# Kernel tuning notes

Measured on AMD Instinct MI355X. Metric: run time of the kernel, lower is better.

The kernel has to match this reference:

```python
import jax, jax.numpy as jnp
import numpy as np

B, N, D = 2, 8192, 1024
H, DH = 8, 64  # heads, dim_head; inner = H*DH = 512
INNER = H * DH


def setup_inputs() -> dict:
    key = jax.random.key(0)
    k1, k2, k3 = jax.random.split(key, 3)
    x = jax.random.normal(k1, (B, N, D), dtype=jnp.float32)
    # xavier_uniform-ish scaling for weights
    W_qkv = jax.random.normal(k2, (D, 3 * INNER), dtype=jnp.float32) * (1.0 / np.sqrt(D))
    W_out = jax.random.normal(k3, (INNER, D), dtype=jnp.float32) * (1.0 / np.sqrt(INNER))
    b_out = jnp.zeros((D,), dtype=jnp.float32)
    return {"x": x, "W_qkv": W_qkv, "W_out": W_out, "b_out": b_out}


def reference(x, W_qkv, W_out, b_out):
    b, n, d = x.shape
    qkv = x @ W_qkv                               # [b, n, 3*inner]
    q, k, v = jnp.split(qkv, 3, axis=-1)          # each [b, n, inner]

    def to_heads(t):
        return t.reshape(b, n, H, DH).transpose(0, 2, 1, 3)  # [b, h, n, dh]

    q, k, v = to_heads(q), to_heads(k), to_heads(v)
    q = jax.nn.softmax(q, axis=-1)                # over dim_head
    k = jax.nn.softmax(k, axis=-2)                # over sequence
    # context: k^T v  -> [b, h, dh, dh]
    context = jnp.einsum('bhnd,bhne->bhde', k, v)
    out = jnp.einsum('bhnd,bhde->bhne', q, context)  # [b, h, n, dh]
    out = out.transpose(0, 2, 1, 3).reshape(b, n, INNER)
    return out @ W_out + b_out                    # [b, n, d]
```

## Files before the change

### kernel.cpp

```cpp
#include <hip/hip_runtime.h>
#include <stdint.h>


typedef _Float16 half4 __attribute__((ext_vector_type(4)));
typedef _Float16 half8 __attribute__((ext_vector_type(8)));
typedef float f32x4 __attribute__((ext_vector_type(4)));

#define WS_XB 0UL
#define WS_WQKVT 33554432UL
#define WS_CWT 37748736UL
#define WS_EKH 54525952UL
#define WS_VH 71303168UL
#define WS_SQ 88080384UL
#define WS_CTXPART 104857600UL
#define WS_COLPART 113246208UL

__device__ __forceinline__ void gld16(const void* g, void* l) {
  __builtin_amdgcn_global_load_lds(
      (const __attribute__((address_space(1))) unsigned int*)g,
      (__attribute__((address_space(3))) unsigned int*)l, 16, 0, 0);
}

__global__ void prep_kernel(const float* __restrict__ x,
                            const float* __restrict__ Wqkv,
                            _Float16* __restrict__ xb,
                            _Float16* __restrict__ wqkvT) {
  const int blk = blockIdx.x;
  if (blk < 16384) {
    int i = blk * 256 + threadIdx.x;
    f32x4 v = *(const f32x4*)(x + (size_t)i * 4);
    half4 h = {(_Float16)v[0], (_Float16)v[1], (_Float16)v[2], (_Float16)v[3]};
    *(half4*)(xb + (size_t)i * 4) = h;
  } else {
    int i = (blk - 16384) * 256 + threadIdx.x;
    int c = i >> 10, r = i & 1023;
    wqkvT[i] = (_Float16)Wqkv[(size_t)r * 1536 + c];
  }
}


__device__ __forceinline__ void stage_tile(const _Float16* __restrict__ G, int K,
                                           int rowbase, int kt, char* region,
                                           int t) {
  char* wbase = region + (t & ~63) * 16;
#pragma unroll
  for (int q = 0; q < 4; ++q) {
    const int row = q * 32 + (t >> 3);
    const int col8 = ((t & 7) ^ (row & 7)) * 8;
    gld16(G + (size_t)(rowbase + row) * K + kt + col8, wbase + q * 4096);
  }
}

template <int EPI>
__global__ __launch_bounds__(256, 2) void gemm128(
    const _Float16* __restrict__ A, const _Float16* __restrict__ BT, int K,
    int NTN, int bstride, _Float16* __restrict__ oQ, _Float16* __restrict__ oK,
    _Float16* __restrict__ oV, float* __restrict__ oC,
    const float* __restrict__ bias) {
  __shared__ char lds[65536];
  const int t = threadIdx.x;
  const int l = t & 63, w = t >> 6;
  const int wm = w >> 1, wn = w & 1;
  const int fr = l & 15, qq = l >> 4;
  const int swzx = (fr & 7) << 4;

  const int nwg = gridDim.x;
  const int cpx = nwg >> 3;
  const int wg = (blockIdx.x & 7) * cpx + (blockIdx.x >> 3);
  const int tileM = wg / NTN, tileN = wg - tileM * NTN;
  const int mbase = tileM * 128, nbase = tileN * 128;
  BT += (size_t)(tileM >> 6) * bstride;

  const int NT = K >> 6;
  f32x4 acc[4][4] = {};
  half8 a[4][2], b[4][2];

  auto STG = [&](int tile) {
    int kt = tile * 64;
    if (kt > K - 64) kt = K - 64;
    char* base = lds + ((tile & 1) << 15);
    stage_tile(A, K, mbase, kt, base, t);
    stage_tile(BT, K, nbase, kt, base + 16384, t);
  };

  STG(0);
  STG(1);
  asm volatile("s_waitcnt vmcnt(8)" ::: "memory");
  __builtin_amdgcn_s_barrier();

  for (int t2 = 0; t2 < NT; ++t2) {
    const char* ldsA = lds + ((t2 & 1) << 15);
    const char* ldsB = ldsA + 16384;
    STG(t2 + 1);
#pragma unroll
    for (int mi = 0; mi < 4; ++mi)
#pragma unroll
      for (int kk = 0; kk < 2; ++kk) {
        int off = (wm * 64 + mi * 16 + fr) * 128 + ((kk * 64 + qq * 16) ^ swzx);
        a[mi][kk] = *(const half8*)(ldsA + off);
      }
#pragma unroll
    for (int ni = 0; ni < 4; ++ni)
#pragma unroll
      for (int kk = 0; kk < 2; ++kk) {
        int off = (wn * 64 + ni * 16 + fr) * 128 + ((kk * 64 + qq * 16) ^ swzx);
        b[ni][kk] = *(const half8*)(ldsB + off);
      }
    __builtin_amdgcn_s_barrier();
    __builtin_amdgcn_s_setprio(1);
#pragma unroll
    for (int mi = 0; mi < 4; ++mi)
#pragma unroll
      for (int ni = 0; ni < 2; ++ni)
#pragma unroll
        for (int kk = 0; kk < 2; ++kk)
          acc[mi][ni] = __builtin_amdgcn_mfma_f32_16x16x32_f16(
              a[mi][kk], b[ni][kk], acc[mi][ni], 0, 0, 0);
    __builtin_amdgcn_s_setprio(0);
    asm volatile("s_waitcnt vmcnt(0) lgkmcnt(0)" ::: "memory");
    __builtin_amdgcn_s_barrier();
    __builtin_amdgcn_s_setprio(1);
#pragma unroll
    for (int mi = 0; mi < 4; ++mi)
#pragma unroll
      for (int ni = 2; ni < 4; ++ni)
#pragma unroll
        for (int kk = 0; kk < 2; ++kk)
          acc[mi][ni] = __builtin_amdgcn_mfma_f32_16x16x32_f16(
              a[mi][kk], b[ni][kk], acc[mi][ni], 0, 0, 0);
    __builtin_amdgcn_s_setprio(0);
  }

  if (EPI == 0) {
    const int gcol0 = nbase + wn * 64;
    const int which = gcol0 >> 9;
    if (which == 0) {
#pragma unroll
      for (int mi = 0; mi < 4; ++mi) {
        const int grow = mbase + wm * 64 + mi * 16 + qq * 4;
        float e[4][4], rs[4];
#pragma unroll
        for (int r = 0; r < 4; ++r) {
          float s = 0.f;
#pragma unroll
          for (int ni = 0; ni < 4; ++ni) {
            e[ni][r] = __expf(acc[mi][ni][r]);
            s += e[ni][r];
          }
#pragma unroll
          for (int off = 1; off < 16; off <<= 1) s += __shfl_xor(s, off, 64);
          rs[r] = 1.f / s;
        }
#pragma unroll
        for (int ni = 0; ni < 4; ++ni) {
          const int gcol = gcol0 + ni * 16 + fr;
#pragma unroll
          for (int r = 0; r < 4; ++r)
            oQ[(size_t)(grow + r) * 512 + gcol] = (_Float16)(e[ni][r] * rs[r]);
        }
      }
    } else {
      _Float16* dst0 = (which == 1) ? oK : oV;
      const int h = (gcol0 >> 6) & 7;
#pragma unroll
      for (int mi = 0; mi < 4; ++mi) {
        const int grow = mbase + wm * 64 + mi * 16 + qq * 4;
        const int bidx = grow >> 13, n = grow & 8191;
        const size_t rb = ((size_t)((bidx << 3) + h) * 8192 + n) * 64;
#pragma unroll
        for (int ni = 0; ni < 4; ++ni) {
          const int d = ni * 16 + fr;
#pragma unroll
          for (int r = 0; r < 4; ++r) {
            float v = acc[mi][ni][r];
            if (which == 1) v = __expf(v);
            dst0[rb + (size_t)r * 64 + d] = (_Float16)v;
          }
        }
      }
    }
  } else {
#pragma unroll
    for (int mi = 0; mi < 4; ++mi) {
      const int grow = mbase + wm * 64 + mi * 16 + qq * 4;
#pragma unroll
      for (int ni = 0; ni < 4; ++ni) {
        const int gcol = nbase + wn * 64 + ni * 16 + fr;
        const float bb = bias[gcol];
#pragma unroll
        for (int r = 0; r < 4; ++r)
          oC[(size_t)(grow + r) * 1024 + gcol] = acc[mi][ni][r] + bb;
      }
    }
  }
}

__global__ __launch_bounds__(256, 2) void ctx_partial_kernel(
    const _Float16* __restrict__ ekh, const _Float16* __restrict__ vh,
    float* __restrict__ ctxpart, float* __restrict__ colpart) {
  __shared__ char smem[65536];
  __shared__ float credu[4][64];
  _Float16* sek = (_Float16*)smem;
  _Float16* svv = (_Float16*)(smem + 32768);
  const int t = threadIdx.x, l = t & 63, w = t >> 6;
  const int bh = blockIdx.x >> 5, ch = blockIdx.x & 31;
  const size_t rowbase = ((size_t)bh * 8192 + ch * 256) * 64;
  {
    const char* eksrc = (const char*)(ekh + rowbase);
    const char* vsrc = (const char*)(vh + rowbase);
    char* ekbase = smem + w * 1024;
    char* vbase = smem + 32768 + w * 1024;
#pragma unroll
    for (int s = 0; s < 8; ++s) {
      gld16(eksrc + (size_t)(s * 256 + t) * 16, ekbase + s * 4096);
      gld16(vsrc + (size_t)(s * 256 + t) * 16, vbase + s * 4096);
    }
  }
  asm volatile("s_waitcnt vmcnt(0)" ::: "memory");
  __builtin_amdgcn_s_barrier();

  const int d0 = (l & 7) * 8, e0 = (l >> 3) * 8;
  f32x4 acc[8][2] = {};
  float cacc[8] = {};
  const int n0 = w * 64;
  for (int n = n0; n < n0 + 64; ++n) {
    half8 k8 = *(const half8*)&sek[n * 64 + d0];
    half8 v8 = *(const half8*)&svv[n * 64 + e0];
    float e[8];
    f32x4 v4[2];
#pragma unroll
    for (int i = 0; i < 8; ++i) e[i] = (float)k8[i];
#pragma unroll
    for (int j = 0; j < 8; ++j) v4[j >> 2][j & 3] = (float)v8[j];
#pragma unroll
    for (int i = 0; i < 8; ++i) {
      cacc[i] += e[i];
      acc[i][0] += v4[0] * e[i];
      acc[i][1] += v4[1] * e[i];
    }
  }
  __builtin_amdgcn_s_barrier();
  float* red = (float*)smem;
#pragma unroll
  for (int i = 0; i < 8; ++i) {
    *(f32x4*)&red[w * 4096 + (d0 + i) * 64 + e0] = acc[i][0];
    *(f32x4*)&red[w * 4096 + (d0 + i) * 64 + e0 + 4] = acc[i][1];
  }
  if (l < 8) {
#pragma unroll
    for (int i = 0; i < 8; ++i) credu[w][l * 8 + i] = cacc[i];
  }
  __syncthreads();
  float* cp = ctxpart + (size_t)blockIdx.x * 4096;
#pragma unroll
  for (int s = 0; s < 4; ++s) {
    const int r = t * 16 + s * 4;
    f32x4 sum = *(const f32x4*)&red[r];
    sum += *(const f32x4*)&red[4096 + r];
    sum += *(const f32x4*)&red[8192 + r];
    sum += *(const f32x4*)&red[12288 + r];
    *(f32x4*)&cp[r] = sum;
  }
  if (t < 64)
    colpart[blockIdx.x * 64 + t] =
        credu[0][t] + credu[1][t] + credu[2][t] + credu[3][t];
}

__global__ __launch_bounds__(256) void ctxw_kernel(
    const float* __restrict__ ctxpart, const float* __restrict__ colpart,
    const float* __restrict__ Wout, _Float16* __restrict__ cwT) {
  __shared__ float part[4][64];
  __shared__ float csp[32];
  __shared__ float crow[64];
  const int blk = blockIdx.x;
  const int bh = blk >> 6, d = blk & 63;
  const int b = bh >> 3, h = bh & 7;
  const int t = threadIdx.x;
  const int e = t & 63, cq = t >> 6;
  float p = 0.f;
#pragma unroll
  for (int cc = 0; cc < 8; ++cc)
    p += ctxpart[(size_t)(bh * 32 + cq * 8 + cc) * 4096 + d * 64 + e];
  part[cq][e] = p;
  if (t >= 64 && t < 96)
    csp[t - 64] = colpart[(size_t)(bh * 32 + (t - 64)) * 64 + d];
  __syncthreads();
  if (t < 64) {
    float csum = 0.f;
#pragma unroll
    for (int c = 0; c < 32; ++c) csum += csp[c];
    crow[t] = (part[0][t] + part[1][t] + part[2][t] + part[3][t]) / csum;
  }
  __syncthreads();
  float acc[4] = {};
  for (int e2 = 0; e2 < 64; ++e2) {
    const float c = crow[e2];
    const float* wr = Wout + (size_t)(h * 64 + e2) * 1024 + t;
#pragma unroll
    for (int j = 0; j < 4; ++j) acc[j] += c * wr[j * 256];
  }
  _Float16* dst = cwT + (size_t)b * 524288 + (size_t)t * 512 + h * 64 + d;
#pragma unroll
  for (int j = 0; j < 4; ++j) dst[(size_t)j * 256 * 512] = (_Float16)acc[j];
}

extern "C" void kernel_launch(void* const* d_in, const int* in_sizes, int n_in,
                              void* d_out, int out_size, void* d_ws, size_t ws_size,
                              hipStream_t stream) {
  const float* x = (const float*)d_in[0];
  const float* Wqkv = (const float*)d_in[1];
  const float* Wout = (const float*)d_in[2];
  const float* bout = (const float*)d_in[3];
  float* out = (float*)d_out;
  char* ws = (char*)d_ws;

  _Float16* xb = (_Float16*)(ws + WS_XB);
  _Float16* wqkvT = (_Float16*)(ws + WS_WQKVT);
  _Float16* cwT = (_Float16*)(ws + WS_CWT);
  _Float16* ekh = (_Float16*)(ws + WS_EKH);
  _Float16* vh = (_Float16*)(ws + WS_VH);
  _Float16* sq = (_Float16*)(ws + WS_SQ);
  float* ctxpart = (float*)(ws + WS_CTXPART);
  float* colpart = (float*)(ws + WS_COLPART);

  prep_kernel<<<22528, 256, 0, stream>>>(x, Wqkv, xb, wqkvT);
  gemm128<0><<<1536, 256, 0, stream>>>(xb, wqkvT, 1024, 12, 0, sq, ekh, vh,
                                       nullptr, nullptr);
  ctx_partial_kernel<<<512, 256, 0, stream>>>(ekh, vh, ctxpart, colpart);
  ctxw_kernel<<<1024, 256, 0, stream>>>(ctxpart, colpart, Wout, cwT);
  gemm128<1><<<1024, 256, 0, stream>>>(sq, cwT, 512, 8, 524288, nullptr,
                                       nullptr, nullptr, out, bout);
}
```

Before: 162.6 us.

## Fuse K^T V context partials into QKV GEMM epilogue

```diff
diff --git a/kernel.cpp b/kernel.cpp
--- a/kernel.cpp
+++ b/kernel.cpp
@@ -9,11 +9,9 @@
 #define WS_XB 0UL
 #define WS_WQKVT 33554432UL
 #define WS_CWT 37748736UL
-#define WS_EKH 54525952UL
-#define WS_VH 71303168UL
+#define WS_CTXPART 54525952UL
+#define WS_COLPART 71303168UL
 #define WS_SQ 88080384UL
-#define WS_CTXPART 104857600UL
-#define WS_COLPART 113246208UL
 
 __device__ __forceinline__ void gld16(const void* g, void* l) {
   __builtin_amdgcn_global_load_lds(
@@ -51,12 +49,24 @@
   }
 }
 
+__device__ __forceinline__ void stage_tile64(const _Float16* __restrict__ G,
+                                             int K, int rowbase, int kt,
+                                             char* region, int t) {
+  char* wbase = region + (t & ~63) * 16;
+#pragma unroll
+  for (int q = 0; q < 2; ++q) {
+    const int row = q * 32 + (t >> 3);
+    const int col8 = ((t & 7) ^ (row & 7)) * 8;
+    gld16(G + (size_t)(rowbase + row) * K + kt + col8, wbase + q * 4096);
+  }
+}
+
 template <int EPI>
 __global__ __launch_bounds__(256, 2) void gemm128(
     const _Float16* __restrict__ A, const _Float16* __restrict__ BT, int K,
-    int NTN, int bstride, _Float16* __restrict__ oQ, _Float16* __restrict__ oK,
-    _Float16* __restrict__ oV, float* __restrict__ oC,
-    const float* __restrict__ bias) {
+    int NTN, int bstride, _Float16* __restrict__ oQ,
+    float* __restrict__ ctxpart, float* __restrict__ colpart,
+    float* __restrict__ oC, const float* __restrict__ bias) {
   __shared__ char lds[65536];
   const int t = threadIdx.x;
   const int l = t & 63, w = t >> 6;
@@ -80,7 +90,13 @@
     if (kt > K - 64) kt = K - 64;
     char* base = lds + ((tile & 1) << 15);
     stage_tile(A, K, mbase, kt, base, t);
-    stage_tile(BT, K, nbase, kt, base + 16384, t);
+    if (EPI == 1 || tileN < 4) {
+      stage_tile(BT, K, nbase, kt, base + 16384, t);
+    } else {
+      const int h = tileN - 4;
+      stage_tile64(BT, K, 512 + h * 64, kt, base + 16384, t);
+      stage_tile64(BT, K, 1024 + h * 64, kt, base + 16384 + 8192, t);
+    }
   };
 
   STG(0);
@@ -132,9 +148,8 @@
   }
 
   if (EPI == 0) {
-    const int gcol0 = nbase + wn * 64;
-    const int which = gcol0 >> 9;
-    if (which == 0) {
+    if (tileN < 4) {
+      const int gcol0 = nbase + wn * 64;
 #pragma unroll
       for (int mi = 0; mi < 4; ++mi) {
         const int grow = mbase + wm * 64 + mi * 16 + qq * 4;
@@ -160,24 +175,44 @@
         }
       }
     } else {
-      _Float16* dst0 = (which == 1) ? oK : oV;
-      const int h = (gcol0 >> 6) & 7;
+      const int h = tileN - 4;
+      float* sf = (float*)lds;
 #pragma unroll
       for (int mi = 0; mi < 4; ++mi) {
-        const int grow = mbase + wm * 64 + mi * 16 + qq * 4;
-        const int bidx = grow >> 13, n = grow & 8191;
-        const size_t rb = ((size_t)((bidx << 3) + h) * 8192 + n) * 64;
+        const int n = wm * 64 + mi * 16 + qq * 4;
 #pragma unroll
         for (int ni = 0; ni < 4; ++ni) {
-          const int d = ni * 16 + fr;
+          const int c = wn * 64 + ni * 16 + fr;
 #pragma unroll
           for (int r = 0; r < 4; ++r) {
             float v = acc[mi][ni][r];
-            if (which == 1) v = __expf(v);
-            dst0[rb + (size_t)r * 64 + d] = (_Float16)v;
+            if (wn == 0) v = __expf(v);
+            sf[(size_t)(n + r) * 128 + c] = v;
           }
         }
       }
+      __syncthreads();
+      const int d0 = (t & 15) * 4, e0 = (t >> 4) * 4;
+      f32x4 cacc = {0.f, 0.f, 0.f, 0.f};
+      float pacc[4][4] = {};
+      for (int n = 0; n < 128; ++n) {
+        f32x4 ek4 = *(const f32x4*)&sf[(size_t)n * 128 + d0];
+        f32x4 vv4 = *(const f32x4*)&sf[(size_t)n * 128 + 64 + e0];
+        cacc += ek4;
+#pragma unroll
+        for (int i = 0; i < 4; ++i)
+#pragma unroll
+          for (int j = 0; j < 4; ++j) pacc[i][j] += ek4[i] * vv4[j];
+      }
+      const int bh = (tileM >> 6) * 8 + h, chunk = tileM & 63;
+      float* cp = ctxpart + ((size_t)bh * 64 + chunk) * 4096;
+#pragma unroll
+      for (int i = 0; i < 4; ++i) {
+        f32x4 o = {pacc[i][0], pacc[i][1], pacc[i][2], pacc[i][3]};
+        *(f32x4*)&cp[(d0 + i) * 64 + e0] = o;
+      }
+      if (t < 16)
+        *(f32x4*)&colpart[((size_t)bh * 64 + chunk) * 64 + d0] = cacc;
     }
   } else {
 #pragma unroll
@@ -193,84 +228,13 @@
       }
     }
   }
-}
-
-__global__ __launch_bounds__(256, 2) void ctx_partial_kernel(
-    const _Float16* __restrict__ ekh, const _Float16* __restrict__ vh,
-    float* __restrict__ ctxpart, float* __restrict__ colpart) {
-  __shared__ char smem[65536];
-  __shared__ float credu[4][64];
-  _Float16* sek = (_Float16*)smem;
-  _Float16* svv = (_Float16*)(smem + 32768);
-  const int t = threadIdx.x, l = t & 63, w = t >> 6;
-  const int bh = blockIdx.x >> 5, ch = blockIdx.x & 31;
-  const size_t rowbase = ((size_t)bh * 8192 + ch * 256) * 64;
-  {
-    const char* eksrc = (const char*)(ekh + rowbase);
-    const char* vsrc = (const char*)(vh + rowbase);
-    char* ekbase = smem + w * 1024;
-    char* vbase = smem + 32768 + w * 1024;
-#pragma unroll
-    for (int s = 0; s < 8; ++s) {
-      gld16(eksrc + (size_t)(s * 256 + t) * 16, ekbase + s * 4096);
-      gld16(vsrc + (size_t)(s * 256 + t) * 16, vbase + s * 4096);
-    }
-  }
-  asm volatile("s_waitcnt vmcnt(0)" ::: "memory");
-  __builtin_amdgcn_s_barrier();
-
-  const int d0 = (l & 7) * 8, e0 = (l >> 3) * 8;
-  f32x4 acc[8][2] = {};
-  float cacc[8] = {};
-  const int n0 = w * 64;
-  for (int n = n0; n < n0 + 64; ++n) {
-    half8 k8 = *(const half8*)&sek[n * 64 + d0];
-    half8 v8 = *(const half8*)&svv[n * 64 + e0];
-    float e[8];
-    f32x4 v4[2];
-#pragma unroll
-    for (int i = 0; i < 8; ++i) e[i] = (float)k8[i];
-#pragma unroll
-    for (int j = 0; j < 8; ++j) v4[j >> 2][j & 3] = (float)v8[j];
-#pragma unroll
-    for (int i = 0; i < 8; ++i) {
-      cacc[i] += e[i];
-      acc[i][0] += v4[0] * e[i];
-      acc[i][1] += v4[1] * e[i];
-    }
-  }
-  __builtin_amdgcn_s_barrier();
-  float* red = (float*)smem;
-#pragma unroll
-  for (int i = 0; i < 8; ++i) {
-    *(f32x4*)&red[w * 4096 + (d0 + i) * 64 + e0] = acc[i][0];
-    *(f32x4*)&red[w * 4096 + (d0 + i) * 64 + e0 + 4] = acc[i][1];
-  }
-  if (l < 8) {
-#pragma unroll
-    for (int i = 0; i < 8; ++i) credu[w][l * 8 + i] = cacc[i];
-  }
-  __syncthreads();
-  float* cp = ctxpart + (size_t)blockIdx.x * 4096;
-#pragma unroll
-  for (int s = 0; s < 4; ++s) {
-    const int r = t * 16 + s * 4;
-    f32x4 sum = *(const f32x4*)&red[r];
-    sum += *(const f32x4*)&red[4096 + r];
-    sum += *(const f32x4*)&red[8192 + r];
-    sum += *(const f32x4*)&red[12288 + r];
-    *(f32x4*)&cp[r] = sum;
-  }
-  if (t < 64)
-    colpart[blockIdx.x * 64 + t] =
-        credu[0][t] + credu[1][t] + credu[2][t] + credu[3][t];
 }
 
 __global__ __launch_bounds__(256) void ctxw_kernel(
     const float* __restrict__ ctxpart, const float* __restrict__ colpart,
     const float* __restrict__ Wout, _Float16* __restrict__ cwT) {
   __shared__ float part[4][64];
-  __shared__ float csp[32];
+  __shared__ float csp[64];
   __shared__ float crow[64];
   const int blk = blockIdx.x;
   const int bh = blk >> 6, d = blk & 63;
@@ -279,16 +243,16 @@
   const int e = t & 63, cq = t >> 6;
   float p = 0.f;
 #pragma unroll
-  for (int cc = 0; cc < 8; ++cc)
-    p += ctxpart[(size_t)(bh * 32 + cq * 8 + cc) * 4096 + d * 64 + e];
+  for (int cc = 0; cc < 16; ++cc)
+    p += ctxpart[((size_t)bh * 64 + cq * 16 + cc) * 4096 + d * 64 + e];
   part[cq][e] = p;
-  if (t >= 64 && t < 96)
-    csp[t - 64] = colpart[(size_t)(bh * 32 + (t - 64)) * 64 + d];
+  if (t >= 64 && t < 128)
+    csp[t - 64] = colpart[((size_t)bh * 64 + (t - 64)) * 64 + d];
   __syncthreads();
   if (t < 64) {
     float csum = 0.f;
 #pragma unroll
-    for (int c = 0; c < 32; ++c) csum += csp[c];
+    for (int c = 0; c < 64; ++c) csum += csp[c];
     crow[t] = (part[0][t] + part[1][t] + part[2][t] + part[3][t]) / csum;
   }
   __syncthreads();
@@ -317,16 +281,13 @@
   _Float16* xb = (_Float16*)(ws + WS_XB);
   _Float16* wqkvT = (_Float16*)(ws + WS_WQKVT);
   _Float16* cwT = (_Float16*)(ws + WS_CWT);
-  _Float16* ekh = (_Float16*)(ws + WS_EKH);
-  _Float16* vh = (_Float16*)(ws + WS_VH);
   _Float16* sq = (_Float16*)(ws + WS_SQ);
   float* ctxpart = (float*)(ws + WS_CTXPART);
   float* colpart = (float*)(ws + WS_COLPART);
 
   prep_kernel<<<22528, 256, 0, stream>>>(x, Wqkv, xb, wqkvT);
-  gemm128<0><<<1536, 256, 0, stream>>>(xb, wqkvT, 1024, 12, 0, sq, ekh, vh,
-                                       nullptr, nullptr);
-  ctx_partial_kernel<<<512, 256, 0, stream>>>(ekh, vh, ctxpart, colpart);
+  gemm128<0><<<1536, 256, 0, stream>>>(xb, wqkvT, 1024, 12, 0, sq, ctxpart,
+                                       colpart, nullptr, nullptr);
   ctxw_kernel<<<1024, 256, 0, stream>>>(ctxpart, colpart, Wout, cwT);
   gemm128<1><<<1024, 256, 0, stream>>>(sq, cwT, 512, 8, 524288, nullptr,
                                        nullptr, nullptr, out, bout);
```

Result: faster. 151.7 us (-6.7%).
